# Optimization experiments

Measured on AMD Instinct MI355X. Metric: run time of the kernel, lower is better.

The kernel has to match this reference:

```python
import jax, jax.numpy as jnp
import numpy as np

N, M, D, IN_DIM, RF_DIM, N_REL, L, NQ = 50000, 800000, 64, 768, 768, 500, 2, 2048


def _leaky(x):
    return jnp.where(x >= 0, x, 0.01 * x)  # nn.LeakyReLU default slope


def _ln(x, g, b):
    mu = jnp.mean(x, axis=-1, keepdims=True)
    var = jnp.mean(jnp.square(x - mu), axis=-1, keepdims=True)
    return (x - mu) / jnp.sqrt(var + 1e-5) * g + b


def setup_inputs() -> dict:
    key = jax.random.key(0)
    ks = jax.random.split(key, 24)
    ht = jax.random.randint(ks[0], (M, 2), 0, N)
    # ensure every node receives >= 1 message (avoids 0/0 NaN, as real batches do)
    ht = ht.at[:N, 0].set(jnp.arange(N))
    r_tensor = jax.random.randint(ks[1], (M,), 0, N_REL)
    entity_feat = jax.random.normal(ks[2], (N, IN_DIM), dtype=jnp.float32)
    queries = jnp.zeros((M,), jnp.int32).at[:NQ].set(1)
    s = 0.02
    rel_table = jax.random.normal(ks[3], (N_REL, RF_DIM), dtype=jnp.float32)  # frozen
    inp = {
        "ht": ht, "r_tensor": r_tensor, "entity_feat": entity_feat, "queries": queries,
        "rel_table": rel_table,
        "W_ent": s * jax.random.normal(ks[4], (IN_DIM, D)), "b_ent": jnp.zeros((D,)),
        "g_ent": jnp.ones((D,)), "be_ent": jnp.zeros((D,)),
        "W_edge_in": s * jax.random.normal(ks[5], (RF_DIM, D)), "b_edge_in": jnp.zeros((D,)),
        "g_edge": jnp.ones((D,)), "be_edge": jnp.zeros((D,)),
        "mp_Wf": s * jax.random.normal(ks[6], (L, 2 * D, D)), "mp_bf": jnp.zeros((L, D)),
        "mp_Wb": s * jax.random.normal(ks[7], (L, 2 * D, D)), "mp_bb": jnp.zeros((L, D)),
        "mp_g": jnp.ones((L, D)), "mp_be": jnp.zeros((L, D)),
        "eu_W": s * jax.random.normal(ks[8], (L, 3 * D, D)), "eu_b": jnp.zeros((L, D)),
        "eu_g": jnp.ones((L, D)), "eu_be": jnp.zeros((L, D)),
        "cls_W1": s * jax.random.normal(ks[9], (6 * D, D)), "cls_b1": jnp.zeros((D,)),
        "cls_W2": s * jax.random.normal(ks[10], (D, 1)), "cls_b2": jnp.zeros((1,)),
    }
    return inp


def _forward(ht, r_tensor, queries, rel_table, entity_feat,
             W_ent, b_ent, g_ent, be_ent, W_edge_in, b_edge_in, g_edge, be_edge,
             mp_Wf, mp_bf, mp_Wb, mp_bb, mp_g, mp_be,
             eu_W, eu_b, eu_g, eu_be, cls_W1, cls_b1, cls_W2, cls_b2):
    H0 = _ln(_leaky(entity_feat @ W_ent + b_ent), g_ent, be_ent)      # n x d
    r_embed = rel_table[r_tensor]                                     # m x rf
    E0 = _ln(_leaky(r_embed @ W_edge_in + b_edge_in), g_edge, be_edge)  # m x d
    H, E = H0, E0
    heads, tails = ht[:, 0], ht[:, 1]
    dst = jnp.concatenate([tails, heads])                             # 2m
    ones = jnp.ones((2 * M,), H.dtype)
    cnt = jax.ops.segment_sum(ones, dst, num_segments=N)              # per-node msg count
    for l in range(L):
        # message calculation (fwd uses head reps, back uses tail reps)
        mf = jnp.concatenate([H[heads], E], axis=1) @ mp_Wf[l] + mp_bf[l]
        mb = jnp.concatenate([H[tails], E], axis=1) @ mp_Wb[l] + mp_bb[l]
        msgs = jnp.concatenate([mf, mb], axis=0)                      # 2m x d
        agg = jax.ops.segment_sum(msgs, dst, num_segments=N) / cnt[:, None]
        H = _ln(_leaky(agg) + H, mp_g[l], mp_be[l])
        # edge update
        triple = jnp.concatenate([H[heads], E, H[tails]], axis=1)     # m x 3d
        E = _ln(_leaky(triple @ eu_W[l] + eu_b[l]) + E, eu_g[l], eu_be[l])
    # triple classification on query edges
    qi = jnp.nonzero(queries, size=NQ)[0]
    htq = ht[qi]
    feat = jnp.concatenate([E[qi], E0[qi], H[htq[:, 0]], H0[htq[:, 0]],
                            H[htq[:, 1]], H0[htq[:, 1]]], axis=1)     # NQ x 6d
    out = _leaky(feat @ cls_W1 + cls_b1) @ cls_W2 + cls_b2            # NQ x 1
    return out


def reference(ht, r_tensor, entity_feat, queries, rel_table,
              W_ent, b_ent, g_ent, be_ent, W_edge_in, b_edge_in, g_edge, be_edge,
              mp_Wf, mp_bf, mp_Wb, mp_bb, mp_g, mp_be,
              eu_W, eu_b, eu_g, eu_be, cls_W1, cls_b1, cls_W2, cls_b2):
    return _forward(ht, r_tensor, queries, rel_table, entity_feat,
                    W_ent, b_ent, g_ent, be_ent, W_edge_in, b_edge_in, g_edge, be_edge,
                    mp_Wf, mp_bf, mp_Wb, mp_bb, mp_g, mp_be,
                    eu_W, eu_b, eu_g, eu_be, cls_W1, cls_b1, cls_W2, cls_b2)
```

## Files before the change

### kernel.cpp

```cpp
#include <hip/hip_runtime.h>
#include <hip/hip_bf16.h>
#include <cstdint>

constexpr int IN_DIM = 768;
constexpr int FB_ENT = 0;
constexpr int FB_L0  = 96;
constexpr int FB_L1  = 128;
constexpr int NFRAG  = 160;

typedef __attribute__((ext_vector_type(8))) short bf16x8;
typedef __attribute__((ext_vector_type(4))) float f32x4;

static __device__ __forceinline__ float leaky_(float x){ return x >= 0.0f ? x : 0.01f * x; }

static __device__ __forceinline__ float wsum_(float v){
#pragma unroll
  for (int m = 1; m < 64; m <<= 1) v += __shfl_xor(v, m, 64);
  return v;
}

static __device__ __forceinline__ float wln_(float v, float g, float be){
  float mu  = wsum_(v) * 0.015625f;
  float c   = v - mu;
  float var = wsum_(c * c) * 0.015625f;
  return c * rsqrtf(var + 1e-5f) * g + be;
}

template<int CTRL>
static __device__ __forceinline__ float dpp_radd(float x){
  const int t = __builtin_amdgcn_update_dpp(0, __float_as_int(x), CTRL, 0xf, 0xf, true);
  return x + __int_as_float(t);
}
static __device__ __forceinline__ float rowsum16_(float x){
  x = dpp_radd<0x121>(x);
  x = dpp_radd<0x122>(x);
  x = dpp_radd<0x124>(x);
  x = dpp_radd<0x128>(x);
  return x;
}

static __device__ __forceinline__ unsigned short f2bf(float x){
  return __bfloat16_as_ushort(__float2bfloat16(x));
}
static __device__ __forceinline__ float bf2f(unsigned short u){
  return __bfloat162float(__ushort_as_bfloat16(u));
}
static __device__ __forceinline__ void split4(const float4 a, ushort4& hi, ushort4& lo){
  hi.x = f2bf(a.x); lo.x = f2bf(a.x - bf2f(hi.x));
  hi.y = f2bf(a.y); lo.y = f2bf(a.y - bf2f(hi.y));
  hi.z = f2bf(a.z); lo.z = f2bf(a.z - bf2f(hi.z));
  hi.w = f2bf(a.w); lo.w = f2bf(a.w - bf2f(hi.w));
}

static __device__ __forceinline__ f32x4 mfma3(bf16x8 ah, bf16x8 al, bf16x8 wh, bf16x8 wl, f32x4 acc){
  acc = __builtin_amdgcn_mfma_f32_16x16x32_bf16(ah, wh, acc, 0, 0, 0);
  acc = __builtin_amdgcn_mfma_f32_16x16x32_bf16(al, wh, acc, 0, 0, 0);
  acc = __builtin_amdgcn_mfma_f32_16x16x32_bf16(ah, wl, acc, 0, 0, 0);
  return acc;
}

__global__ __launch_bounds__(256) void k_wprep(
    const float* __restrict__ Went, const float* __restrict__ Wf,
    const float* __restrict__ Wb,
    unsigned short* __restrict__ Fhi, unsigned short* __restrict__ Flo)
{
  const int gt = blockIdx.x * 256 + threadIdx.x;
  if (gt >= NFRAG * 64) return;
  const int fid = gt >> 6, lane = gt & 63;
  int kind, lf;
  if (fid < FB_L0)      { kind = 0; lf = fid; }
  else if (fid < FB_L1) { kind = 1; lf = fid - FB_L0; }
  else                  { kind = 2; lf = fid - FB_L1; }
  const int kt = lf >> 2, nn = lf & 3;
  const int col = nn * 16 + (lane & 15);
  const int r0  = kt * 32 + (lane >> 4) * 8;
  unsigned short* ph = Fhi + ((size_t)fid << 9) + lane * 8;
  unsigned short* pl = Flo + ((size_t)fid << 9) + lane * 8;
#pragma unroll
  for (int j = 0; j < 8; ++j){
    const int gr = r0 + j;
    const float* rp;
    if (kind == 0)      rp = Went + (size_t)gr * 64;
    else if (kind == 1) rp = (gr < 128) ? Wf + (size_t)gr * 64
                                        : Wb + (size_t)(gr - 128) * 64;
    else                rp = (gr < 128) ? Wf + (size_t)(128 + gr) * 64
                                        : Wb + (size_t)gr * 64;
    const float v = rp[col];
    const unsigned short h = f2bf(v);
    ph[j] = h;
    pl[j] = f2bf(v - bf2f(h));
  }
}

__global__ __launch_bounds__(256) void k_encm(const float* __restrict__ X,
    const unsigned short* __restrict__ Fhi, const unsigned short* __restrict__ Flo,
    const float* __restrict__ b, const float* __restrict__ g_,
    const float* __restrict__ be, float* __restrict__ o0, float* __restrict__ o1, int nrows)
{
  __shared__ unsigned short Ahi[64 * 128];
  __shared__ unsigned short Alo[64 * 128];
  const int tile = blockIdx.x * 64;
  const int tid = threadIdx.x;
  const int w = tid >> 6, lane = tid & 63, g = lane >> 4, lr = lane & 15;
  const int rowb = w * 16;

  f32x4 acc[4];
#pragma unroll
  for (int n = 0; n < 4; ++n){
    const float bv = b[n * 16 + lr];
    acc[n] = (f32x4){bv, bv, bv, bv};
  }

  for (int ch = 0; ch < 6; ++ch){
    __syncthreads();
#pragma unroll
    for (int i = 0; i < 8; ++i){
      const int idx = tid + 256 * i;
      const int row = idx >> 5, c = idx & 31;
      int gr = tile + row; if (gr >= nrows) gr = nrows - 1;
      const float4 a = *(const float4*)&X[(size_t)gr * IN_DIM + ch * 128 + c * 4];
      ushort4 hi, lo; split4(a, hi, lo);
      const int ad = (row * 256 + c * 8) ^ ((row & 7) << 4);
      *(ushort4*)((char*)Ahi + ad) = hi;
      *(ushort4*)((char*)Alo + ad) = lo;
    }
    __syncthreads();

    bf16x8 Ah[4], Al[4];
#pragma unroll
    for (int kt = 0; kt < 4; ++kt){
      const int row = rowb + lr;
      const int ad = (row * 256 + kt * 64 + g * 16) ^ ((row & 7) << 4);
      Ah[kt] = *(const bf16x8*)((const char*)Ahi + ad);
      Al[kt] = *(const bf16x8*)((const char*)Alo + ad);
    }
    const int fb = ch * 16;
#pragma unroll
    for (int n = 0; n < 4; ++n)
#pragma unroll
      for (int kt = 0; kt < 4; ++kt){
        const size_t fo = (((size_t)(fb + kt * 4 + n)) << 9) + lane * 8;
        acc[n] = mfma3(Ah[kt], Al[kt], *(const bf16x8*)(Fhi + fo), *(const bf16x8*)(Flo + fo), acc[n]);
      }
  }

#pragma unroll
  for (int reg = 0; reg < 4; ++reg){
    const int lrow = rowb + g * 4 + reg;
    float v[4];
#pragma unroll
    for (int n = 0; n < 4; ++n) v[n] = leaky_(acc[n][reg]);
    float s = v[0] + v[1] + v[2] + v[3];
#pragma unroll
    for (int msk = 1; msk < 16; msk <<= 1) s += __shfl_xor(s, msk, 64);
    const float mu = s * 0.015625f;
    float q = 0.f;
#pragma unroll
    for (int n = 0; n < 4; ++n){ v[n] -= mu; q += v[n] * v[n]; }
#pragma unroll
    for (int msk = 1; msk < 16; msk <<= 1) q += __shfl_xor(q, msk, 64);
    const float rs = rsqrtf(q * 0.015625f + 1e-5f);
    const int r = tile + lrow;
    if (r < nrows){
#pragma unroll
      for (int n = 0; n < 4; ++n){
        const int col = n * 16 + lr;
        const float o = v[n] * rs * g_[col] + be[col];
        o0[(size_t)r * 64 + col] = o;
        o1[(size_t)r * 64 + col] = o;
      }
    }
  }
}

__global__ __launch_bounds__(256) void k_hupd2m(float* __restrict__ H,
    const float* __restrict__ Sall,
    const int* __restrict__ cf, const int* __restrict__ cb,
    const unsigned short* __restrict__ Fhi, const unsigned short* __restrict__ Flo, int fb,
    const float* __restrict__ bf, const float* __restrict__ bb,
    const float* __restrict__ g_, const float* __restrict__ be, int N)
{
  __shared__ unsigned short Ahi[64 * 256];
  __shared__ unsigned short Alo[64 * 256];
  const int tile = blockIdx.x * 64, tid = threadIdx.x;
#pragma unroll
  for (int i = 0; i < 16; ++i){
    const int idx = tid + 256 * i;
    const int row = idx >> 6, c = idx & 63;
    int gr = tile + row; if (gr >= N) gr = N - 1;
    const float4 a = *(const float4*)&Sall[(size_t)gr * 256 + c * 4];
    ushort4 hi, lo; split4(a, hi, lo);
    const int ad = (row * 512 + c * 8) ^ ((row & 7) << 4);
    *(ushort4*)((char*)Ahi + ad) = hi;
    *(ushort4*)((char*)Alo + ad) = lo;
  }
  __syncthreads();

  const int w = tid >> 6, lane = tid & 63, g = lane >> 4, lr = lane & 15;
  const int rowb = w * 16;
  bf16x8 Ah[8], Al[8];
#pragma unroll
  for (int kt = 0; kt < 8; ++kt){
    const int row = rowb + lr;
    const int ad = (row * 512 + kt * 64 + g * 16) ^ ((row & 7) << 4);
    Ah[kt] = *(const bf16x8*)((const char*)Ahi + ad);
    Al[kt] = *(const bf16x8*)((const char*)Alo + ad);
  }

  int cfv[4], cbv[4];
#pragma unroll
  for (int reg = 0; reg < 4; ++reg){
    int r = tile + rowb + g * 4 + reg; if (r >= N) r = N - 1;
    cfv[reg] = cf[r]; cbv[reg] = cb[r];
  }
  f32x4 acc[4];
#pragma unroll
  for (int n = 0; n < 4; ++n){
    const float bfc = bf[n * 16 + lr], bbc = bb[n * 16 + lr];
#pragma unroll
    for (int reg = 0; reg < 4; ++reg)
      acc[n][reg] = (float)cfv[reg] * bfc + (float)cbv[reg] * bbc;
  }
#pragma unroll
  for (int n = 0; n < 4; ++n)
#pragma unroll
    for (int kt = 0; kt < 8; ++kt){
      const size_t fo = (((size_t)(fb + kt * 4 + n)) << 9) + lane * 8;
      acc[n] = mfma3(Ah[kt], Al[kt], *(const bf16x8*)(Fhi + fo), *(const bf16x8*)(Flo + fo), acc[n]);
    }

#pragma unroll
  for (int reg = 0; reg < 4; ++reg){
    const int lrow = rowb + g * 4 + reg;
    const int r = tile + lrow;
    const int rr = (r < N) ? r : N - 1;
    const float c = (float)(cfv[reg] + cbv[reg]);
    float v[4];
#pragma unroll
    for (int n = 0; n < 4; ++n)
      v[n] = leaky_(acc[n][reg] / c) + H[(size_t)rr * 64 + n * 16 + lr];
    float s = v[0] + v[1] + v[2] + v[3];
#pragma unroll
    for (int msk = 1; msk < 16; msk <<= 1) s += __shfl_xor(s, msk, 64);
    const float mu = s * 0.015625f;
    float q = 0.f;
#pragma unroll
    for (int n = 0; n < 4; ++n){ v[n] -= mu; q += v[n] * v[n]; }
#pragma unroll
    for (int msk = 1; msk < 16; msk <<= 1) q += __shfl_xor(q, msk, 64);
    const float rs = rsqrtf(q * 0.015625f + 1e-5f);
    if (r < N){
#pragma unroll
      for (int n = 0; n < 4; ++n){
        const int col = n * 16 + lr;
        H[(size_t)r * 64 + col] = v[n] * rs * g_[col] + be[col];
      }
    }
  }
}

__global__ __launch_bounds__(256) void k_enc(const float* __restrict__ X,
    const float* __restrict__ W, const float* __restrict__ b,
    const float* __restrict__ g, const float* __restrict__ be,
    float* __restrict__ o0, float* __restrict__ o1, int nrows)
{
  const int w = threadIdx.x >> 6, d = threadIdx.x & 63;
  const int rbase = blockIdx.x * 16 + w * 4;
  int rows[4];
#pragma unroll
  for (int j = 0; j < 4; ++j){ int r = rbase + j; rows[j] = r < nrows ? r : nrows - 1; }
  float acc[4] = {0.f, 0.f, 0.f, 0.f};
  for (int k4 = 0; k4 < IN_DIM / 4; ++k4){
    const int k = k4 * 4;
    const float w0 = W[(k+0)*64+d], w1 = W[(k+1)*64+d];
    const float w2 = W[(k+2)*64+d], w3 = W[(k+3)*64+d];
#pragma unroll
    for (int j = 0; j < 4; ++j){
      const float4 a = *(const float4*)&X[(size_t)rows[j] * IN_DIM + k];
      acc[j] = fmaf(a.x, w0, fmaf(a.y, w1, fmaf(a.z, w2, fmaf(a.w, w3, acc[j]))));
    }
  }
#pragma unroll
  for (int j = 0; j < 4; ++j){
    const int r = rbase + j;
    if (r < nrows){
      float v = wln_(leaky_(acc[j] + b[d]), g[d], be[d]);
      o0[(size_t)r*64+d] = v;
      if (o1) o1[(size_t)r*64+d] = v;
    }
  }
}

__global__ __launch_bounds__(256) void k_xw2(const float* __restrict__ X,
    const float* __restrict__ W1, const float* __restrict__ W3,
    float* __restrict__ Y, int nrows)
{
  const int w = threadIdx.x >> 6, d = threadIdx.x & 63;
  const int rbase = blockIdx.x * 16 + w * 4;
  int rows[4];
#pragma unroll
  for (int j = 0; j < 4; ++j){ int r = rbase + j; rows[j] = r < nrows ? r : nrows - 1; }
  float a1[4] = {0.f,0.f,0.f,0.f}, a3[4] = {0.f,0.f,0.f,0.f};
  for (int k4 = 0; k4 < 16; ++k4){
    const int k = k4 * 4;
    const float u0 = W1[(k+0)*64+d], u1 = W1[(k+1)*64+d];
    const float u2 = W1[(k+2)*64+d], u3 = W1[(k+3)*64+d];
    const float v0 = W3[(k+0)*64+d], v1 = W3[(k+1)*64+d];
    const float v2 = W3[(k+2)*64+d], v3 = W3[(k+3)*64+d];
#pragma unroll
    for (int j = 0; j < 4; ++j){
      const float4 a = *(const float4*)&X[(size_t)rows[j] * 64 + k];
      a1[j] = fmaf(a.x, u0, fmaf(a.y, u1, fmaf(a.z, u2, fmaf(a.w, u3, a1[j]))));
      a3[j] = fmaf(a.x, v0, fmaf(a.y, v1, fmaf(a.z, v2, fmaf(a.w, v3, a3[j]))));
    }
  }
#pragma unroll
  for (int j = 0; j < 4; ++j){
    const int r = rbase + j;
    if (r < nrows){
      Y[(size_t)r * 128 + d]      = a1[j];
      Y[(size_t)r * 128 + 64 + d] = a3[j];
    }
  }
}

__global__ __launch_bounds__(256) void k_tep(const float* __restrict__ E0t,
    const float* __restrict__ W, const float* __restrict__ bias,
    float2* __restrict__ TEP, int nrows)
{
  const int w = threadIdx.x >> 6, d = threadIdx.x & 63;
  const int rbase = blockIdx.x * 16 + w * 4;
  int rows[4];
#pragma unroll
  for (int j = 0; j < 4; ++j){ int r = rbase + j; rows[j] = r < nrows ? r : nrows - 1; }
  const float b0 = bias[d];
  float acc[4] = {b0, b0, b0, b0};
  for (int k4 = 0; k4 < 16; ++k4){
    const int k = k4 * 4;
    const float w0 = W[(k+0)*64+d], w1 = W[(k+1)*64+d];
    const float w2 = W[(k+2)*64+d], w3 = W[(k+3)*64+d];
#pragma unroll
    for (int j = 0; j < 4; ++j){
      const float4 a = *(const float4*)&E0t[(size_t)rows[j] * 64 + k];
      acc[j] = fmaf(a.x, w0, fmaf(a.y, w1, fmaf(a.z, w2, fmaf(a.w, w3, acc[j]))));
    }
  }
#pragma unroll
  for (int j = 0; j < 4; ++j){
    const int r = rbase + j;
    if (r < nrows) TEP[(size_t)r * 64 + d] = make_float2(acc[j], E0t[(size_t)r * 64 + d]);
  }
}

__global__ __launch_bounds__(256) void k_cnt(const int* __restrict__ ht,
    int* __restrict__ cf, int* __restrict__ cb, int M)
{
  int m = blockIdx.x * 256 + threadIdx.x;
  if (m < M){
    atomicAdd(&cf[ht[2*m+1]], 1);
    atomicAdd(&cb[ht[2*m+0]], 1);
  }
}

__global__ __launch_bounds__(256) void k_scan1(const int* __restrict__ cf,
    const int* __restrict__ cb, int* __restrict__ pos, int* __restrict__ bsum, int N)
{
  __shared__ int ws[4];
  const int tid = threadIdx.x, lane = tid & 63, w = tid >> 6;
  const int i = blockIdx.x * 256 + tid;
  const int v = (i < N) ? (cf[i] + cb[i]) : 0;
  int inc = v;
#pragma unroll
  for (int off = 1; off < 64; off <<= 1){
    int t = __shfl_up(inc, off, 64);
    if (lane >= off) inc += t;
  }
  if (lane == 63) ws[w] = inc;
  __syncthreads();
  int wbase = 0;
  for (int j = 0; j < w; ++j) wbase += ws[j];
  if (i < N) pos[i] = wbase + inc - v;
  if (tid == 255) bsum[blockIdx.x] = wbase + inc;
}

__global__ __launch_bounds__(256) void k_scan3(int* __restrict__ pos,
    const int* __restrict__ bsum, int N)
{
  const int i = blockIdx.x * 256 + threadIdx.x;
  if (i < N) pos[i] += bsum[blockIdx.x];
}

__global__ __launch_bounds__(256) void k_qscan(int* __restrict__ bcnt, int nb)
{
  __shared__ int ws[4];
  const int tid = threadIdx.x, lane = tid & 63, w = tid >> 6;
  const int chunk = (nb + 255) / 256;
  int s = 0;
  for (int i = 0; i < chunk; ++i){ int idx = tid * chunk + i; if (idx < nb) s += bcnt[idx]; }
  int v = s;
#pragma unroll
  for (int off = 1; off < 64; off <<= 1){ int t = __shfl_up(v, off, 64); if (lane >= off) v += t; }
  if (lane == 63) ws[w] = v;
  __syncthreads();
  int wbase = 0;
  for (int i = 0; i < w; ++i) wbase += ws[i];
  int run = wbase + v - s;
  for (int i = 0; i < chunk; ++i){
    int idx = tid * chunk + i;
    if (idx < nb){ int t = bcnt[idx]; bcnt[idx] = run; run += t; }
  }
}

__global__ __launch_bounds__(256) void k_slot(const int* __restrict__ ht,
    const int* __restrict__ rt, int* __restrict__ pos,
    int2* __restrict__ si, int M)
{
  const int j = blockIdx.x * 256 + threadIdx.x;
  if (j < 2 * M){
    const int fwd = (j < M) ? 1 : 0;
    const int e = fwd ? j : j - M;
    const int dst = fwd ? ht[2*e+1] : ht[2*e];
    const int src = fwd ? ht[2*e]   : ht[2*e+1];
    const int slot = atomicAdd(&pos[dst], 1);
    si[slot] = make_int2(src | (fwd << 31), rt[e]);
  }
}

static __device__ __forceinline__ void qmerge_(f32x4& a){
#pragma unroll
  for (int c = 0; c < 4; ++c){
    float x = a[c];
    x += __shfl_xor(x, 16, 64);
    x += __shfl_xor(x, 32, 64);
    a[c] = x;
  }
}

__global__ __launch_bounds__(256) void k_sum(const float* __restrict__ H,
    const float* __restrict__ E, const int2* __restrict__ si,
    const int* __restrict__ pos_end,
    const int* __restrict__ cf, const int* __restrict__ cb,
    float* __restrict__ Sall, int N)
{
  const int w = threadIdx.x >> 6, lane = threadIdx.x & 63;
  const int n = blockIdx.x * 4 + w;
  if (n >= N) return;
  const int q = lane >> 4, l16 = lane & 15;
  const int end = pos_end[n];
  const int start = end - (cf[n] + cb[n]);
  f32x4 sf = {0,0,0,0}, ef = {0,0,0,0}, sb = {0,0,0,0}, eb = {0,0,0,0};
#pragma unroll 2
  for (int i0 = start; i0 < end; i0 += 4){
    int i = i0 + q;
    const bool act = (i < end); if (!act) i = end - 1;
    const int2 sv = si[i];
    const unsigned u = (unsigned)sv.x;
    const int src = (int)(u & 0x7fffffffu);
    const bool fwd = (u >> 31) != 0;
    const float4 h4 = *(const float4*)&H[(size_t)src * 64 + l16 * 4];
    const float4 e4 = *(const float4*)&E[(size_t)sv.y * 64 + l16 * 4];
    const float pf = (act && fwd) ? 1.f : 0.f;
    const float pb = (act && !fwd) ? 1.f : 0.f;
    sf[0] = fmaf(pf, h4.x, sf[0]); sf[1] = fmaf(pf, h4.y, sf[1]);
    sf[2] = fmaf(pf, h4.z, sf[2]); sf[3] = fmaf(pf, h4.w, sf[3]);
    ef[0] = fmaf(pf, e4.x, ef[0]); ef[1] = fmaf(pf, e4.y, ef[1]);
    ef[2] = fmaf(pf, e4.z, ef[2]); ef[3] = fmaf(pf, e4.w, ef[3]);
    sb[0] = fmaf(pb, h4.x, sb[0]); sb[1] = fmaf(pb, h4.y, sb[1]);
    sb[2] = fmaf(pb, h4.z, sb[2]); sb[3] = fmaf(pb, h4.w, sb[3]);
    eb[0] = fmaf(pb, e4.x, eb[0]); eb[1] = fmaf(pb, e4.y, eb[1]);
    eb[2] = fmaf(pb, e4.z, eb[2]); eb[3] = fmaf(pb, e4.w, eb[3]);
  }
  qmerge_(sf); qmerge_(ef); qmerge_(sb); qmerge_(eb);
  if (q == 0){
    float* S = Sall + (size_t)n * 256;
    *(f32x4*)&S[      l16 * 4] = sf;
    *(f32x4*)&S[ 64 + l16 * 4] = ef;
    *(f32x4*)&S[128 + l16 * 4] = sb;
    *(f32x4*)&S[192 + l16 * 4] = eb;
  }
}

__global__ __launch_bounds__(256) void k_sum2(const float* __restrict__ H,
    const float* __restrict__ HWp, const float2* __restrict__ TEP,
    const int2* __restrict__ si, const int* __restrict__ pos_end,
    const int* __restrict__ cf, const int* __restrict__ cb,
    const float* __restrict__ g0, const float* __restrict__ be0,
    float* __restrict__ Sall, int N)
{
  const int w = threadIdx.x >> 6, lane = threadIdx.x & 63;
  const int n = blockIdx.x * 4 + w;
  if (n >= N) return;
  const int q = lane >> 4, l16 = lane & 15;
  const int end = pos_end[n];
  const int start = end - (cf[n] + cb[n]);
  const float4 gg4  = *(const float4*)&g0 [l16 * 4];
  const float4 bb4  = *(const float4*)&be0[l16 * 4];
  const float4 h1n4 = *(const float4*)&HWp[(size_t)n * 128 +      l16 * 4];
  const float4 h3n4 = *(const float4*)&HWp[(size_t)n * 128 + 64 + l16 * 4];
  f32x4 sf = {0,0,0,0}, ef = {0,0,0,0}, sb = {0,0,0,0}, eb = {0,0,0,0};
#pragma unroll 2
  for (int i0 = start; i0 < end; i0 += 4){
    int i = i0 + q;
    const bool act = (i < end); if (!act) i = end - 1;
    const int2 sv = si[i];
    const unsigned u = (unsigned)sv.x;
    const int src = (int)(u & 0x7fffffffu);
    const bool fwd = (u >> 31) != 0;
    const float4 h4 = *(const float4*)&H[(size_t)src * 64 + l16 * 4];
    const float4 o4 = *(const float4*)&HWp[(size_t)src * 128 + (fwd ? 0 : 64) + l16 * 4];
    const float* tp = (const float*)&TEP[(size_t)sv.y * 64 + l16 * 4];
    const float4 t0 = *(const float4*)&tp[0];
    const float4 t1 = *(const float4*)&tp[4];
    float v[4];
    {
      const float n0 = fwd ? h3n4.x : h1n4.x;
      const float n1 = fwd ? h3n4.y : h1n4.y;
      const float n2 = fwd ? h3n4.z : h1n4.z;
      const float n3 = fwd ? h3n4.w : h1n4.w;
      v[0] = leaky_(o4.x + n0 + t0.x) + t0.y;
      v[1] = leaky_(o4.y + n1 + t0.z) + t0.w;
      v[2] = leaky_(o4.z + n2 + t1.x) + t1.y;
      v[3] = leaky_(o4.w + n3 + t1.z) + t1.w;
    }
    float s  = (v[0] + v[1]) + (v[2] + v[3]);
    float qq = fmaf(v[0], v[0], v[1] * v[1]) + fmaf(v[2], v[2], v[3] * v[3]);
    s  = rowsum16_(s);
    qq = rowsum16_(qq);
    const float mu  = s * 0.015625f;
    const float var = fmaxf(qq * 0.015625f - mu * mu, 0.f);
    const float rsg = rsqrtf(var + 1e-5f);
    float e1[4];
#pragma unroll
    for (int c = 0; c < 4; ++c)
      e1[c] = (v[c] - mu) * rsg * ((const float*)&gg4)[c] + ((const float*)&bb4)[c];
    const float pf = (act && fwd) ? 1.f : 0.f;
    const float pb = (act && !fwd) ? 1.f : 0.f;
    sf[0] = fmaf(pf, h4.x, sf[0]); sf[1] = fmaf(pf, h4.y, sf[1]);
    sf[2] = fmaf(pf, h4.z, sf[2]); sf[3] = fmaf(pf, h4.w, sf[3]);
    ef[0] = fmaf(pf, e1[0], ef[0]); ef[1] = fmaf(pf, e1[1], ef[1]);
    ef[2] = fmaf(pf, e1[2], ef[2]); ef[3] = fmaf(pf, e1[3], ef[3]);
    sb[0] = fmaf(pb, h4.x, sb[0]); sb[1] = fmaf(pb, h4.y, sb[1]);
    sb[2] = fmaf(pb, h4.z, sb[2]); sb[3] = fmaf(pb, h4.w, sb[3]);
    eb[0] = fmaf(pb, e1[0], eb[0]); eb[1] = fmaf(pb, e1[1], eb[1]);
    eb[2] = fmaf(pb, e1[2], eb[2]); eb[3] = fmaf(pb, e1[3], eb[3]);
  }
  qmerge_(sf); qmerge_(ef); qmerge_(sb); qmerge_(eb);
  if (q == 0){
    float* S = Sall + (size_t)n * 256;
    *(f32x4*)&S[      l16 * 4] = sf;
    *(f32x4*)&S[ 64 + l16 * 4] = ef;
    *(f32x4*)&S[128 + l16 * 4] = sb;
    *(f32x4*)&S[192 + l16 * 4] = eb;
  }
}

__global__ __launch_bounds__(256) void k_eu2q(const float* __restrict__ HWp,
    const float2* __restrict__ TEP, const int* __restrict__ ht,
    const int* __restrict__ rt, const int* __restrict__ qi,
    const float* __restrict__ g, const float* __restrict__ be,
    float* __restrict__ e1q, int NQ)
{
  const int w = threadIdx.x >> 6, lane = threadIdx.x & 63;
  const int row = blockIdx.x * 4 + w;
  if (row >= NQ) return;
  const int m = qi[row];
  const int h = ht[2*m], t = ht[2*m+1], r = rt[m];
  const float2 te = TEP[(size_t)r * 64 + lane];
  float v = HWp[(size_t)h*128+lane] + HWp[(size_t)t*128+64+lane] + te.x;
  v = leaky_(v) + te.y;
  e1q[(size_t)row*64+lane] = wln_(v, g[lane], be[lane]);
}

__global__ __launch_bounds__(256) void k_qcount(const int* __restrict__ q,
                                                int* __restrict__ bcnt, int M)
{
  const int j = blockIdx.x * 256 + threadIdx.x;
  const int have = (j < M) && (q[j] != 0);
  unsigned long long bal = __ballot(have);
  if ((threadIdx.x & 63) == 0) atomicAdd(&bcnt[blockIdx.x], (int)__popcll(bal));
}

__global__ __launch_bounds__(256) void k_qemit(const int* __restrict__ q,
    const int* __restrict__ bcnt, int* __restrict__ qi, int M, int NQ)
{
  __shared__ int wb[4];
  const int j = blockIdx.x * 256 + threadIdx.x;
  const int lane = threadIdx.x & 63, w = threadIdx.x >> 6;
  const int have = (j < M) && (q[j] != 0);
  unsigned long long bal = __ballot(have);
  if (lane == 0) wb[w] = (int)__popcll(bal);
  __syncthreads();
  int base = bcnt[blockIdx.x];
  for (int i = 0; i < w; ++i) base += wb[i];
  const int rank = base + (int)__popcll(bal & ((1ull << lane) - 1ull));
  if (have && rank < NQ) qi[rank] = j;
}

__global__ __launch_bounds__(256) void k_feat(
    const float* __restrict__ H, const float* __restrict__ H0,
    const float* __restrict__ e1q, const float* __restrict__ E0t,
    const int* __restrict__ rt, const int* __restrict__ ht, const int* __restrict__ qi,
    const float* __restrict__ W, const float* __restrict__ b,
    const float* __restrict__ g, const float* __restrict__ be,
    float* __restrict__ feat, int NQ)
{
  const int w = threadIdx.x >> 6, d = threadIdx.x & 63;
  const int row = blockIdx.x * 4 + w;
  if (row >= NQ) return;
  const int m = qi[row];
  const int h = ht[2*m], t = ht[2*m+1], r = rt[m];
  const float* seg0 = H   + (size_t)h * 64;
  const float* seg1 = e1q + (size_t)row * 64;
  const float* seg2 = H   + (size_t)t * 64;
  float acc = b[d];
  for (int k4 = 0; k4 < 48; ++k4){
    const int k = k4 * 4;
    const float* A = (k4 < 16) ? seg0 : (k4 < 32) ? seg1 - 64 : seg2 - 128;
    const float4 a = *(const float4*)&A[k];
    acc = fmaf(a.x, W[(k+0)*64+d], fmaf(a.y, W[(k+1)*64+d],
          fmaf(a.z, W[(k+2)*64+d], fmaf(a.w, W[(k+3)*64+d], acc))));
  }
  const float ep = seg1[d];
  const float e2 = wln_(leaky_(acc) + ep, g[d], be[d]);
  float* F = feat + (size_t)row * 384;
  F[      d] = e2;
  F[ 64 + d] = E0t[(size_t)r*64+d];
  F[128 + d] = H [(size_t)h*64+d];
  F[192 + d] = H0[(size_t)h*64+d];
  F[256 + d] = H [(size_t)t*64+d];
  F[320 + d] = H0[(size_t)t*64+d];
}

__global__ __launch_bounds__(256) void k_cls(const float* __restrict__ feat,
    const float* __restrict__ W1, const float* __restrict__ b1,
    const float* __restrict__ W2, const float* __restrict__ b2,
    float* __restrict__ out, int NQ)
{
  const int w = threadIdx.x >> 6, d = threadIdx.x & 63;
  const int row = blockIdx.x * 4 + w;
  if (row >= NQ) return;
  const float* F = feat + (size_t)row * 384;
  float acc = b1[d];
  for (int k4 = 0; k4 < 96; ++k4){
    const int k = k4 * 4;
    const float4 a = *(const float4*)&F[k];
    acc = fmaf(a.x, W1[(k+0)*64+d], fmaf(a.y, W1[(k+1)*64+d],
          fmaf(a.z, W1[(k+2)*64+d], fmaf(a.w, W1[(k+3)*64+d], acc))));
  }
  float hs = leaky_(acc) * W2[d];
  hs = wsum_(hs);
  if (d == 0) out[row] = hs + b2[0];
}

extern "C" void kernel_launch(void* const* d_in, const int* in_sizes, int n_in,
                              void* d_out, int out_size, void* d_ws, size_t ws_size,
                              hipStream_t stream)
{
  const int*   ht    = (const int*)  d_in[0];
  const int*   rt    = (const int*)  d_in[1];
  const float* ef    = (const float*)d_in[2];
  const int*   q     = (const int*)  d_in[3];
  const float* rtab  = (const float*)d_in[4];
  const float* W_ent = (const float*)d_in[5];
  const float* b_ent = (const float*)d_in[6];
  const float* g_ent = (const float*)d_in[7];
  const float* be_ent= (const float*)d_in[8];
  const float* W_ein = (const float*)d_in[9];
  const float* b_ein = (const float*)d_in[10];
  const float* g_e   = (const float*)d_in[11];
  const float* be_e  = (const float*)d_in[12];
  const float* mp_Wf = (const float*)d_in[13];
  const float* mp_bf = (const float*)d_in[14];
  const float* mp_Wb = (const float*)d_in[15];
  const float* mp_bb = (const float*)d_in[16];
  const float* mp_g  = (const float*)d_in[17];
  const float* mp_be = (const float*)d_in[18];
  const float* eu_W  = (const float*)d_in[19];
  const float* eu_b  = (const float*)d_in[20];
  const float* eu_g  = (const float*)d_in[21];
  const float* eu_be = (const float*)d_in[22];
  const float* clsW1 = (const float*)d_in[23];
  const float* clsb1 = (const float*)d_in[24];
  const float* clsW2 = (const float*)d_in[25];
  const float* clsb2 = (const float*)d_in[26];

  const int M    = in_sizes[1];
  const int N    = in_sizes[2] / IN_DIM;
  const int NREL = in_sizes[4] / IN_DIM;
  const int NQ   = out_size;
  const int nb   = (M + 255) / 256;
  const int nbn  = (N + 255) / 256;

  unsigned short* Fhi = (unsigned short*)d_ws;
  unsigned short* Flo = Fhi + (size_t)NFRAG * 512;
  float* H0    = (float*)(Flo + (size_t)NFRAG * 512);
  float* H     = H0    + (size_t)N * 64;
  float* HWp   = H     + (size_t)N * 64;
  float* Sall  = HWp   + (size_t)N * 128;
  float* E0t   = Sall  + (size_t)N * 256;
  float2* TEP  = (float2*)(E0t + (size_t)NREL * 64);
  float* e1q   = (float*)(TEP + (size_t)NREL * 64);
  float* feat  = e1q   + (size_t)NQ * 64;
  int*   cf    = (int*)(feat + (size_t)NQ * 384);
  int*   cb    = cf + N;
  int*   pos   = cb + N;
  int2*  si    = (int2*)(pos + N);
  int*   qi    = (int*)(si + 2 * (size_t)M);
  int*   bcnt  = qi + NQ;
  int*   bsum  = bcnt + nb;

  hipMemsetAsync(cf,   0, (size_t)N  * 4, stream);
  hipMemsetAsync(cb,   0, (size_t)N  * 4, stream);
  hipMemsetAsync(qi,   0, (size_t)NQ * 4, stream);
  hipMemsetAsync(bcnt, 0, (size_t)nb * 4, stream);

  k_wprep<<<(NFRAG * 64 + 255) / 256, 256, 0, stream>>>(W_ent, mp_Wf, mp_Wb, Fhi, Flo);
  k_cnt<<<(M + 255) / 256, 256, 0, stream>>>(ht, cf, cb, M);
  k_scan1<<<nbn, 256, 0, stream>>>(cf, cb, pos, bsum, N);
  k_qscan<<<1, 256, 0, stream>>>(bsum, nbn);
  k_scan3<<<nbn, 256, 0, stream>>>(pos, bsum, N);
  k_slot<<<(2 * M + 255) / 256, 256, 0, stream>>>(ht, rt, pos, si, M);

  k_encm<<<(N + 63) / 64, 256, 0, stream>>>(ef, Fhi, Flo, b_ent, g_ent, be_ent, H0, H, N);
  k_enc<<<(NREL + 15) / 16, 256, 0, stream>>>(rtab, W_ein, b_ein, g_e, be_e, E0t, nullptr, NREL);
  k_tep<<<(NREL + 15) / 16, 256, 0, stream>>>(E0t, eu_W + 64 * 64, eu_b, TEP, NREL);

  const int sgrid = (N + 3) / 4;
  k_sum<<<sgrid, 256, 0, stream>>>(H, E0t, si, pos, cf, cb, Sall, N);
  k_hupd2m<<<(N + 63) / 64, 256, 0, stream>>>(H, Sall, cf, cb, Fhi, Flo, FB_L0,
      mp_bf, mp_bb, mp_g, mp_be, N);
  k_xw2<<<(N + 15) / 16, 256, 0, stream>>>(H, eu_W, eu_W + 128 * 64, HWp, N);

  k_sum2<<<sgrid, 256, 0, stream>>>(H, HWp, TEP, si, pos, cf, cb,
      eu_g, eu_be, Sall, N);

  k_qcount<<<nb, 256, 0, stream>>>(q, bcnt, M);
  k_qscan<<<1, 256, 0, stream>>>(bcnt, nb);
  k_qemit<<<nb, 256, 0, stream>>>(q, bcnt, qi, M, NQ);
  k_eu2q<<<(NQ + 3) / 4, 256, 0, stream>>>(HWp, TEP, ht, rt, qi,
      eu_g, eu_be, e1q, NQ);

  k_hupd2m<<<(N + 63) / 64, 256, 0, stream>>>(H, Sall, cf, cb, Fhi, Flo, FB_L1,
      mp_bf + 64, mp_bb + 64, mp_g + 64, mp_be + 64, N);

  k_feat<<<(NQ + 3) / 4, 256, 0, stream>>>(H, H0, e1q, E0t, rt, ht, qi,
      eu_W + 192 * 64, eu_b + 64, eu_g + 64, eu_be + 64, feat, NQ);
  k_cls<<<(NQ + 3) / 4, 256, 0, stream>>>(feat, clsW1, clsb1, clsW2, clsb2,
      (float*)d_out, NQ);
}
```

Measured before the change: 667.5 us.

## Split incoming-edge CSR into separate forward and backward segments per node

Replaces the single merged per-node edge list, which tagged each entry with a direction bit, by two CSR segments: forward edges grouped by tail and backward edges grouped by head, each with its own scan. The sum kernels now run two direction-specific loops, so each edge does a single predicated accumulation and no longer selects between forward and backward values per lane. k_slot handles both directions of an edge in one thread. In exchange it adds an extra scan pass of three launches, and each node's gather is split into two loops that each carry their own tail padding.

```diff
diff --git a/kernel.cpp b/kernel.cpp
--- a/kernel.cpp
+++ b/kernel.cpp
@@ -362,13 +362,13 @@
   }
 }
 
-__global__ __launch_bounds__(256) void k_scan1(const int* __restrict__ cf,
-    const int* __restrict__ cb, int* __restrict__ pos, int* __restrict__ bsum, int N)
+__global__ __launch_bounds__(256) void k_scan1(const int* __restrict__ c,
+    int* __restrict__ pos, int* __restrict__ bsum, int N)
 {
   __shared__ int ws[4];
   const int tid = threadIdx.x, lane = tid & 63, w = tid >> 6;
   const int i = blockIdx.x * 256 + tid;
-  const int v = (i < N) ? (cf[i] + cb[i]) : 0;
+  const int v = (i < N) ? c[i] : 0;
   int inc = v;
 #pragma unroll
   for (int off = 1; off < 64; off <<= 1){
@@ -384,10 +384,10 @@
 }
 
 __global__ __launch_bounds__(256) void k_scan3(int* __restrict__ pos,
-    const int* __restrict__ bsum, int N)
+    const int* __restrict__ bsum, int N, int offset)
 {
   const int i = blockIdx.x * 256 + threadIdx.x;
-  if (i < N) pos[i] += bsum[blockIdx.x];
+  if (i < N) pos[i] += bsum[blockIdx.x] + offset;
 }
 
 __global__ __launch_bounds__(256) void k_qscan(int* __restrict__ bcnt, int nb)
@@ -412,17 +412,16 @@
 }
 
 __global__ __launch_bounds__(256) void k_slot(const int* __restrict__ ht,
-    const int* __restrict__ rt, int* __restrict__ pos,
+    const int* __restrict__ rt, int* __restrict__ posf, int* __restrict__ posb,
     int2* __restrict__ si, int M)
 {
-  const int j = blockIdx.x * 256 + threadIdx.x;
-  if (j < 2 * M){
-    const int fwd = (j < M) ? 1 : 0;
-    const int e = fwd ? j : j - M;
-    const int dst = fwd ? ht[2*e+1] : ht[2*e];
-    const int src = fwd ? ht[2*e]   : ht[2*e+1];
-    const int slot = atomicAdd(&pos[dst], 1);
-    si[slot] = make_int2(src | (fwd << 31), rt[e]);
+  const int m = blockIdx.x * 256 + threadIdx.x;
+  if (m < M){
+    const int h = ht[2*m], t = ht[2*m+1], r = rt[m];
+    const int sf_ = atomicAdd(&posf[t], 1);
+    si[sf_] = make_int2(h, r);
+    const int sb_ = atomicAdd(&posb[h], 1);
+    si[sb_] = make_int2(t, r);
   }
 }
 
@@ -438,7 +437,7 @@
 
 __global__ __launch_bounds__(256) void k_sum(const float* __restrict__ H,
     const float* __restrict__ E, const int2* __restrict__ si,
-    const int* __restrict__ pos_end,
+    const int* __restrict__ posf_end, const int* __restrict__ posb_end,
     const int* __restrict__ cf, const int* __restrict__ cb,
     float* __restrict__ Sall, int N)
 {
@@ -446,29 +445,38 @@
   const int n = blockIdx.x * 4 + w;
   if (n >= N) return;
   const int q = lane >> 4, l16 = lane & 15;
-  const int end = pos_end[n];
-  const int start = end - (cf[n] + cb[n]);
   f32x4 sf = {0,0,0,0}, ef = {0,0,0,0}, sb = {0,0,0,0}, eb = {0,0,0,0};
+  {
+    const int end = posf_end[n], start = end - cf[n];
 #pragma unroll 2
-  for (int i0 = start; i0 < end; i0 += 4){
-    int i = i0 + q;
-    const bool act = (i < end); if (!act) i = end - 1;
-    const int2 sv = si[i];
-    const unsigned u = (unsigned)sv.x;
-    const int src = (int)(u & 0x7fffffffu);
-    const bool fwd = (u >> 31) != 0;
-    const float4 h4 = *(const float4*)&H[(size_t)src * 64 + l16 * 4];
-    const float4 e4 = *(const float4*)&E[(size_t)sv.y * 64 + l16 * 4];
-    const float pf = (act && fwd) ? 1.f : 0.f;
-    const float pb = (act && !fwd) ? 1.f : 0.f;
-    sf[0] = fmaf(pf, h4.x, sf[0]); sf[1] = fmaf(pf, h4.y, sf[1]);
-    sf[2] = fmaf(pf, h4.z, sf[2]); sf[3] = fmaf(pf, h4.w, sf[3]);
-    ef[0] = fmaf(pf, e4.x, ef[0]); ef[1] = fmaf(pf, e4.y, ef[1]);
-    ef[2] = fmaf(pf, e4.z, ef[2]); ef[3] = fmaf(pf, e4.w, ef[3]);
-    sb[0] = fmaf(pb, h4.x, sb[0]); sb[1] = fmaf(pb, h4.y, sb[1]);
-    sb[2] = fmaf(pb, h4.z, sb[2]); sb[3] = fmaf(pb, h4.w, sb[3]);
-    eb[0] = fmaf(pb, e4.x, eb[0]); eb[1] = fmaf(pb, e4.y, eb[1]);
-    eb[2] = fmaf(pb, e4.z, eb[2]); eb[3] = fmaf(pb, e4.w, eb[3]);
+    for (int i0 = start; i0 < end; i0 += 4){
+      int i = i0 + q;
+      const bool act = (i < end); if (!act) i = end - 1;
+      const int2 sv = si[i];
+      const float4 h4 = *(const float4*)&H[(size_t)sv.x * 64 + l16 * 4];
+      const float4 e4 = *(const float4*)&E[(size_t)sv.y * 64 + l16 * 4];
+      const float p = act ? 1.f : 0.f;
+      sf[0] = fmaf(p, h4.x, sf[0]); sf[1] = fmaf(p, h4.y, sf[1]);
+      sf[2] = fmaf(p, h4.z, sf[2]); sf[3] = fmaf(p, h4.w, sf[3]);
+      ef[0] = fmaf(p, e4.x, ef[0]); ef[1] = fmaf(p, e4.y, ef[1]);
+      ef[2] = fmaf(p, e4.z, ef[2]); ef[3] = fmaf(p, e4.w, ef[3]);
+    }
+  }
+  {
+    const int end = posb_end[n], start = end - cb[n];
+#pragma unroll 2
+    for (int i0 = start; i0 < end; i0 += 4){
+      int i = i0 + q;
+      const bool act = (i < end); if (!act) i = end - 1;
+      const int2 sv = si[i];
+      const float4 h4 = *(const float4*)&H[(size_t)sv.x * 64 + l16 * 4];
+      const float4 e4 = *(const float4*)&E[(size_t)sv.y * 64 + l16 * 4];
+      const float p = act ? 1.f : 0.f;
+      sb[0] = fmaf(p, h4.x, sb[0]); sb[1] = fmaf(p, h4.y, sb[1]);
+      sb[2] = fmaf(p, h4.z, sb[2]); sb[3] = fmaf(p, h4.w, sb[3]);
+      eb[0] = fmaf(p, e4.x, eb[0]); eb[1] = fmaf(p, e4.y, eb[1]);
+      eb[2] = fmaf(p, e4.z, eb[2]); eb[3] = fmaf(p, e4.w, eb[3]);
+    }
   }
   qmerge_(sf); qmerge_(ef); qmerge_(sb); qmerge_(eb);
   if (q == 0){
@@ -482,7 +490,8 @@
 
 __global__ __launch_bounds__(256) void k_sum2(const float* __restrict__ H,
     const float* __restrict__ HWp, const float2* __restrict__ TEP,
-    const int2* __restrict__ si, const int* __restrict__ pos_end,
+    const int2* __restrict__ si,
+    const int* __restrict__ posf_end, const int* __restrict__ posb_end,
     const int* __restrict__ cf, const int* __restrict__ cb,
     const float* __restrict__ g0, const float* __restrict__ be0,
     float* __restrict__ Sall, int N)
@@ -491,59 +500,53 @@
   const int n = blockIdx.x * 4 + w;
   if (n >= N) return;
   const int q = lane >> 4, l16 = lane & 15;
-  const int end = pos_end[n];
-  const int start = end - (cf[n] + cb[n]);
   const float4 gg4  = *(const float4*)&g0 [l16 * 4];
   const float4 bb4  = *(const float4*)&be0[l16 * 4];
   const float4 h1n4 = *(const float4*)&HWp[(size_t)n * 128 +      l16 * 4];
   const float4 h3n4 = *(const float4*)&HWp[(size_t)n * 128 + 64 + l16 * 4];
   f32x4 sf = {0,0,0,0}, ef = {0,0,0,0}, sb = {0,0,0,0}, eb = {0,0,0,0};
-#pragma unroll 2
-  for (int i0 = start; i0 < end; i0 += 4){
-    int i = i0 + q;
-    const bool act = (i < end); if (!act) i = end - 1;
-    const int2 sv = si[i];
-    const unsigned u = (unsigned)sv.x;
-    const int src = (int)(u & 0x7fffffffu);
-    const bool fwd = (u >> 31) != 0;
-    const float4 h4 = *(const float4*)&H[(size_t)src * 64 + l16 * 4];
-    const float4 o4 = *(const float4*)&HWp[(size_t)src * 128 + (fwd ? 0 : 64) + l16 * 4];
-    const float* tp = (const float*)&TEP[(size_t)sv.y * 64 + l16 * 4];
-    const float4 t0 = *(const float4*)&tp[0];
-    const float4 t1 = *(const float4*)&tp[4];
-    float v[4];
-    {
-      const float n0 = fwd ? h3n4.x : h1n4.x;
-      const float n1 = fwd ? h3n4.y : h1n4.y;
-      const float n2 = fwd ? h3n4.z : h1n4.z;
-      const float n3 = fwd ? h3n4.w : h1n4.w;
-      v[0] = leaky_(o4.x + n0 + t0.x) + t0.y;
-      v[1] = leaky_(o4.y + n1 + t0.z) + t0.w;
-      v[2] = leaky_(o4.z + n2 + t1.x) + t1.y;
-      v[3] = leaky_(o4.w + n3 + t1.z) + t1.w;
-    }
-    float s  = (v[0] + v[1]) + (v[2] + v[3]);
-    float qq = fmaf(v[0], v[0], v[1] * v[1]) + fmaf(v[2], v[2], v[3] * v[3]);
-    s  = rowsum16_(s);
-    qq = rowsum16_(qq);
-    const float mu  = s * 0.015625f;
-    const float var = fmaxf(qq * 0.015625f - mu * mu, 0.f);
-    const float rsg = rsqrtf(var + 1e-5f);
-    float e1[4];
-#pragma unroll
-    for (int c = 0; c < 4; ++c)
-      e1[c] = (v[c] - mu) * rsg * ((const float*)&gg4)[c] + ((const float*)&bb4)[c];
-    const float pf = (act && fwd) ? 1.f : 0.f;
-    const float pb = (act && !fwd) ? 1.f : 0.f;
-    sf[0] = fmaf(pf, h4.x, sf[0]); sf[1] = fmaf(pf, h4.y, sf[1]);
-    sf[2] = fmaf(pf, h4.z, sf[2]); sf[3] = fmaf(pf, h4.w, sf[3]);
-    ef[0] = fmaf(pf, e1[0], ef[0]); ef[1] = fmaf(pf, e1[1], ef[1]);
-    ef[2] = fmaf(pf, e1[2], ef[2]); ef[3] = fmaf(pf, e1[3], ef[3]);
-    sb[0] = fmaf(pb, h4.x, sb[0]); sb[1] = fmaf(pb, h4.y, sb[1]);
-    sb[2] = fmaf(pb, h4.z, sb[2]); sb[3] = fmaf(pb, h4.w, sb[3]);
-    eb[0] = fmaf(pb, e1[0], eb[0]); eb[1] = fmaf(pb, e1[1], eb[1]);
-    eb[2] = fmaf(pb, e1[2], eb[2]); eb[3] = fmaf(pb, e1[3], eb[3]);
-  }
+
+#define SUM2_LOOP(POS_END, CNT, OTH_OFF, N0, N1, N2, N3, SACC, EACC)            \
+  {                                                                             \
+    const int end = POS_END[n], start = end - CNT[n];                           \
+    _Pragma("unroll 2")                                                         \
+    for (int i0 = start; i0 < end; i0 += 4){                                    \
+      int i = i0 + q;                                                           \
+      const bool act = (i < end); if (!act) i = end - 1;                        \
+      const int2 sv = si[i];                                                    \
+      const float4 h4 = *(const float4*)&H[(size_t)sv.x * 64 + l16 * 4];        \
+      const float4 o4 = *(const float4*)&HWp[(size_t)sv.x * 128 + OTH_OFF + l16 * 4]; \
+      const float* tp = (const float*)&TEP[(size_t)sv.y * 64 + l16 * 4];        \
+      const float4 t0 = *(const float4*)&tp[0];                                 \
+      const float4 t1 = *(const float4*)&tp[4];                                 \
+      float v[4];                                                               \
+      v[0] = leaky_(o4.x + N0 + t0.x) + t0.y;                                   \
+      v[1] = leaky_(o4.y + N1 + t0.z) + t0.w;                                   \
+      v[2] = leaky_(o4.z + N2 + t1.x) + t1.y;                                   \
+      v[3] = leaky_(o4.w + N3 + t1.z) + t1.w;                                   \
+      float s  = (v[0] + v[1]) + (v[2] + v[3]);                                 \
+      float qq = fmaf(v[0], v[0], v[1] * v[1]) + fmaf(v[2], v[2], v[3] * v[3]); \
+      s  = rowsum16_(s);                                                        \
+      qq = rowsum16_(qq);                                                       \
+      const float mu  = s * 0.015625f;                                          \
+      const float var = fmaxf(qq * 0.015625f - mu * mu, 0.f);                   \
+      const float rsg = rsqrtf(var + 1e-5f);                                    \
+      const float p = act ? 1.f : 0.f;                                          \
+      SACC[0] = fmaf(p, h4.x, SACC[0]); SACC[1] = fmaf(p, h4.y, SACC[1]);       \
+      SACC[2] = fmaf(p, h4.z, SACC[2]); SACC[3] = fmaf(p, h4.w, SACC[3]);       \
+      _Pragma("unroll")                                                         \
+      for (int c = 0; c < 4; ++c){                                              \
+        const float e1 = (v[c] - mu) * rsg * ((const float*)&gg4)[c]            \
+                       + ((const float*)&bb4)[c];                               \
+        EACC[c] = fmaf(p, e1, EACC[c]);                                         \
+      }                                                                         \
+    }                                                                           \
+  }
+
+  SUM2_LOOP(posf_end, cf, 0,  h3n4.x, h3n4.y, h3n4.z, h3n4.w, sf, ef)
+  SUM2_LOOP(posb_end, cb, 64, h1n4.x, h1n4.y, h1n4.z, h1n4.w, sb, eb)
+#undef SUM2_LOOP
+
   qmerge_(sf); qmerge_(ef); qmerge_(sb); qmerge_(eb);
   if (q == 0){
     float* S = Sall + (size_t)n * 256;
@@ -703,11 +706,13 @@
   float* feat  = e1q   + (size_t)NQ * 64;
   int*   cf    = (int*)(feat + (size_t)NQ * 384);
   int*   cb    = cf + N;
-  int*   pos   = cb + N;
-  int2*  si    = (int2*)(pos + N);
+  int*   posf  = cb + N;
+  int*   posb  = posf + N;
+  int2*  si    = (int2*)(posb + N);
   int*   qi    = (int*)(si + 2 * (size_t)M);
   int*   bcnt  = qi + NQ;
-  int*   bsum  = bcnt + nb;
+  int*   bsumf = bcnt + nb;
+  int*   bsumb = bsumf + nbn;
 
   hipMemsetAsync(cf,   0, (size_t)N  * 4, stream);
   hipMemsetAsync(cb,   0, (size_t)N  * 4, stream);
@@ -716,22 +721,25 @@
 
   k_wprep<<<(NFRAG * 64 + 255) / 256, 256, 0, stream>>>(W_ent, mp_Wf, mp_Wb, Fhi, Flo);
   k_cnt<<<(M + 255) / 256, 256, 0, stream>>>(ht, cf, cb, M);
-  k_scan1<<<nbn, 256, 0, stream>>>(cf, cb, pos, bsum, N);
-  k_qscan<<<1, 256, 0, stream>>>(bsum, nbn);
-  k_scan3<<<nbn, 256, 0, stream>>>(pos, bsum, N);
-  k_slot<<<(2 * M + 255) / 256, 256, 0, stream>>>(ht, rt, pos, si, M);
+  k_scan1<<<nbn, 256, 0, stream>>>(cf, posf, bsumf, N);
+  k_qscan<<<1, 256, 0, stream>>>(bsumf, nbn);
+  k_scan3<<<nbn, 256, 0, stream>>>(posf, bsumf, N, 0);
+  k_scan1<<<nbn, 256, 0, stream>>>(cb, posb, bsumb, N);
+  k_qscan<<<1, 256, 0, stream>>>(bsumb, nbn);
+  k_scan3<<<nbn, 256, 0, stream>>>(posb, bsumb, N, M);
+  k_slot<<<(M + 255) / 256, 256, 0, stream>>>(ht, rt, posf, posb, si, M);
 
   k_encm<<<(N + 63) / 64, 256, 0, stream>>>(ef, Fhi, Flo, b_ent, g_ent, be_ent, H0, H, N);
   k_enc<<<(NREL + 15) / 16, 256, 0, stream>>>(rtab, W_ein, b_ein, g_e, be_e, E0t, nullptr, NREL);
   k_tep<<<(NREL + 15) / 16, 256, 0, stream>>>(E0t, eu_W + 64 * 64, eu_b, TEP, NREL);
 
   const int sgrid = (N + 3) / 4;
-  k_sum<<<sgrid, 256, 0, stream>>>(H, E0t, si, pos, cf, cb, Sall, N);
+  k_sum<<<sgrid, 256, 0, stream>>>(H, E0t, si, posf, posb, cf, cb, Sall, N);
   k_hupd2m<<<(N + 63) / 64, 256, 0, stream>>>(H, Sall, cf, cb, Fhi, Flo, FB_L0,
       mp_bf, mp_bb, mp_g, mp_be, N);
   k_xw2<<<(N + 15) / 16, 256, 0, stream>>>(H, eu_W, eu_W + 128 * 64, HWp, N);
 
-  k_sum2<<<sgrid, 256, 0, stream>>>(H, HWp, TEP, si, pos, cf, cb,
+  k_sum2<<<sgrid, 256, 0, stream>>>(H, HWp, TEP, si, posf, posb, cf, cb,
       eu_g, eu_be, Sall, N);
 
   k_qcount<<<nb, 256, 0, stream>>>(q, bcnt, M);
```

Result: no change. 665.1 us (-0.4%).
